# Optimization experiments

Hardware: AMD Instinct MI355X
Metric: run time of the kernel (lower is better)

Reference implementation:

```python
import jax, jax.numpy as jnp
import numpy as np
import math

B, S, D_MODEL, N_HEAD = 4, 2048, 1024, 16
D_K = D_MODEL // N_HEAD
ROPE_THETA = 10000.0


def _rope(x):
    # x: [B, H, S, Dk]; interleaved-pair rotary embedding.
    b, h, s, d = x.shape
    inv_freq = ROPE_THETA ** (-jnp.arange(0, d, 2, dtype=jnp.float32) / d)  # [d/2]
    ang = jnp.arange(s, dtype=jnp.float32)[:, None] * inv_freq[None, :]      # [S, d/2]
    cos, sin = jnp.cos(ang), jnp.sin(ang)
    x1, x2 = x[..., 0::2], x[..., 1::2]
    r1 = x1 * cos - x2 * sin
    r2 = x1 * sin + x2 * cos
    return jnp.stack([r1, r2], axis=-1).reshape(b, h, s, d)


def setup_inputs() -> dict:
    key = jax.random.key(0)
    ks = jax.random.split(key, 7)
    sc = 1.0 / math.sqrt(D_MODEL)
    return {
        "q": jax.random.normal(ks[0], (B, S, D_MODEL), jnp.float32),
        "k": jax.random.normal(ks[1], (B, S, D_MODEL), jnp.float32),
        "v": jax.random.normal(ks[2], (B, S, D_MODEL), jnp.float32),
        "Wq": jax.random.normal(ks[3], (D_MODEL, D_MODEL), jnp.float32) * sc,
        "Wk": jax.random.normal(ks[4], (D_MODEL, D_MODEL), jnp.float32) * sc,
        "Wv": jax.random.normal(ks[5], (D_MODEL, D_MODEL), jnp.float32) * sc,
        "Wo": jax.random.normal(ks[6], (D_MODEL, D_MODEL), jnp.float32) * sc,
    }


def _split(x):
    b, s, d = x.shape
    return x.reshape(b, s, N_HEAD, d // N_HEAD).transpose(0, 2, 1, 3)  # [B,H,S,Dk]


def reference(q, k, v, Wq, Wk, Wv, Wo):
    q = jnp.einsum("bsd,de->bse", q, Wq)
    k = jnp.einsum("bsd,de->bse", k, Wk)
    v = jnp.einsum("bsd,de->bse", v, Wv)
    qh, kh, vh = _split(q), _split(k), _split(v)
    qh, kh = _rope(qh), _rope(kh)
    scale = 1.0 / math.sqrt(D_K)
    score = jnp.einsum("bhqd,bhkd->bhqk", qh, kh) * scale  # [B,H,S,S]
    attn = jax.nn.softmax(score, axis=-1)
    out = jnp.einsum("bhqk,bhkd->bhqd", attn, vh)
    out = out.transpose(0, 2, 1, 3).reshape(q.shape[0], q.shape[1], D_MODEL)
    return jnp.einsum("bsd,de->bse", out, Wo)
```

## Files before the change

### kernel.cpp

```cpp
#include <hip/hip_runtime.h>
#include <stdint.h>

#define Bv 4
#define Sv 2048
#define Dv 1024
#define Hv 16
#define DKv 64
#define BSv (Bv * Sv)

typedef unsigned short u16;
typedef __attribute__((ext_vector_type(8))) short short8;
typedef __attribute__((ext_vector_type(8))) unsigned short u16x8;
typedef __attribute__((ext_vector_type(4))) unsigned short u16x4;
typedef __attribute__((ext_vector_type(4))) float f32x4;
typedef __attribute__((ext_vector_type(16))) float f32x16;

__device__ __forceinline__ u16 f2bf(float f) {
  union { float f; uint32_t u; } x; x.f = f;
  uint32_t r = x.u + 0x7FFFu + ((x.u >> 16) & 1u);
  return (u16)(r >> 16);
}

__device__ __forceinline__ uint32_t cvtpk(float lo, float hi) {
  uint32_t r;
  asm("v_cvt_pk_bf16_f32 %0, %1, %2" : "=v"(r) : "v"(lo), "v"(hi));
  return r;
}

__device__ __forceinline__ void gl_lds16(const void* g, void* l) {
  __builtin_amdgcn_global_load_lds(
      (__attribute__((address_space(1))) void*)g,
      (__attribute__((address_space(3))) void*)l, 16, 0, 0);
}

__device__ __forceinline__ f32x4 mfma16(short8 a, short8 b, f32x4 c) {
  return __builtin_amdgcn_mfma_f32_16x16x32_bf16(a, b, c, 0, 0, 0);
}
__device__ __forceinline__ f32x16 mfma32(short8 a, short8 b, f32x16 c) {
  return __builtin_amdgcn_mfma_f32_32x32x16_bf16(a, b, c, 0, 0, 0);
}

template <int N>
__device__ __forceinline__ void tsync() {
  asm volatile("s_waitcnt vmcnt(%0) lgkmcnt(0)" ::"n"(N) : "memory");
  __builtin_amdgcn_s_barrier();
  __builtin_amdgcn_sched_barrier(0);
}

__global__ __launch_bounds__(256) void conv_wt(
    const float* __restrict__ w0, const float* __restrict__ w1,
    const float* __restrict__ w2, const float* __restrict__ w3,
    u16* __restrict__ t0, u16* __restrict__ t1, u16* __restrict__ t2,
    u16* __restrict__ t3) {
  const float* W = (blockIdx.z == 0) ? w0 : (blockIdx.z == 1 ? w1 : (blockIdx.z == 2 ? w2 : w3));
  u16* T = (blockIdx.z == 0) ? t0 : (blockIdx.z == 1 ? t1 : (blockIdx.z == 2 ? t2 : t3));
  __shared__ u16 tile[64][72];
  int nb = blockIdx.x * 64, kb = blockIdx.y * 64;
  int t = threadIdx.x;
#pragma unroll
  for (int p = 0; p < 4; ++p) {
    int idx = p * 256 + t;
    int r = idx >> 4;
    int c4 = (idx & 15) * 4;
    float4 vv = *(const float4*)(W + (size_t)(kb + r) * Dv + nb + c4);
    tile[c4 + 0][r] = f2bf(vv.x);
    tile[c4 + 1][r] = f2bf(vv.y);
    tile[c4 + 2][r] = f2bf(vv.z);
    tile[c4 + 3][r] = f2bf(vv.w);
  }
  __syncthreads();
#pragma unroll
  for (int p = 0; p < 4; ++p) {
    int idx = p * 256 + t;
    int r = idx >> 4;
    int c4 = (idx & 15) * 4;
    u16x4 o = { tile[r][c4], tile[r][c4 + 1], tile[r][c4 + 2], tile[r][c4 + 3] };
    *(u16x4*)(T + (size_t)(nb + r) * Dv + kb + c4) = o;
  }
}

__global__ __launch_bounds__(256, 2) void gemm_qkv(
    const float* __restrict__ A0, const float* __restrict__ A1, const float* __restrict__ A2,
    const u16* __restrict__ B0, const u16* __restrict__ B1, const u16* __restrict__ B2,
    u16* __restrict__ O0, u16* __restrict__ O1, u16* __restrict__ O2) {
  __shared__ u16 As[2][128 * 64];
  __shared__ u16 Bs[2][128 * 64];
  int z = blockIdx.z;
  const float* A = (z == 0) ? A0 : (z == 1 ? A1 : A2);
  const u16* Bt  = (z == 0) ? B0 : (z == 1 ? B1 : B2);
  u16* Out       = (z == 0) ? O0 : (z == 1 ? O1 : O2);
  int mode = z;

  int tid = threadIdx.x;
  int lane = tid & 63, wid = tid >> 6;
  int quad = lane >> 4, cc = lane & 15;
  int wm = (wid >> 1) * 64, wn = (wid & 1) * 64;
  int m0 = blockIdx.x * 128, n0 = blockIdx.y * 128;

  f32x4 acc[4][4];
#pragma unroll
  for (int mi = 0; mi < 4; ++mi)
#pragma unroll
    for (int ni = 0; ni < 4; ++ni) {
      f32x4 zf = {0.f, 0.f, 0.f, 0.f};
      acc[mi][ni] = zf;
    }

  auto stageB = [&](int ki, int b) {
#pragma unroll
    for (int p = 0; p < 4; ++p) {
      int slot = p * 256 + tid;
      int row = slot >> 3, cl = slot & 7;
      int cg = cl ^ (row & 7);
      gl_lds16(Bt + (size_t)(n0 + row) * Dv + ki * 64 + cg * 8, &Bs[b][slot * 8]);
    }
  };

  float4 fa0[4][2], fa1[4][2];
  auto loadA = [&](int ki, float4 (&fs)[4][2]) {
#pragma unroll
    for (int p = 0; p < 4; ++p) {
      int slot = p * 256 + tid;
      int row = slot >> 3, cl = slot & 7;
      int cg = cl ^ (row & 7);
      const float* g = A + (size_t)(m0 + row) * Dv + ki * 64 + cg * 8;
      fs[p][0] = *(const float4*)g;
      fs[p][1] = *(const float4*)(g + 4);
    }
  };
  auto writeA = [&](int b, const float4 (&fs)[4][2]) {
#pragma unroll
    for (int p = 0; p < 4; ++p) {
      int slot = p * 256 + tid;
      union { uint32_t u[4]; u16x8 s; } o;
      o.u[0] = cvtpk(fs[p][0].x, fs[p][0].y);
      o.u[1] = cvtpk(fs[p][0].z, fs[p][0].w);
      o.u[2] = cvtpk(fs[p][1].x, fs[p][1].y);
      o.u[3] = cvtpk(fs[p][1].z, fs[p][1].w);
      *(u16x8*)&As[b][slot * 8] = o.s;
    }
  };
  auto computeTile = [&](int cur) {
#pragma unroll
    for (int kk = 0; kk < 2; ++kk) {
      short8 af[4], bfr[4];
#pragma unroll
      for (int mi = 0; mi < 4; ++mi) {
        int row = wm + mi * 16 + cc;
        int cg = kk * 4 + quad;
        af[mi] = *(const short8*)&As[cur][row * 64 + (cg ^ (row & 7)) * 8];
      }
#pragma unroll
      for (int ni = 0; ni < 4; ++ni) {
        int row = wn + ni * 16 + cc;
        int cg = kk * 4 + quad;
        bfr[ni] = *(const short8*)&Bs[cur][row * 64 + (cg ^ (row & 7)) * 8];
      }
#pragma unroll
      for (int mi = 0; mi < 4; ++mi)
#pragma unroll
        for (int ni = 0; ni < 4; ++ni)
          acc[mi][ni] = mfma16(af[mi], bfr[ni], acc[mi][ni]);
    }
  };

  loadA(0, fa0); writeA(0, fa0); stageB(0, 0);
  asm volatile("" ::: "memory");
  loadA(1, fa1);

  const int NT = Dv / 64;
#pragma unroll 1
  for (int tt = 0; tt < NT; tt += 2) {
    tsync<8>();
    if (tt + 1 < NT) stageB(tt + 1, 1);
    asm volatile("" ::: "memory");
    if (tt + 2 < NT) loadA(tt + 2, fa0);
    computeTile(0);
    if (tt + 1 < NT) writeA(1, fa1);
    if (tt + 2 < NT) tsync<8>(); else tsync<0>();
    if (tt + 2 < NT) stageB(tt + 2, 0);
    asm volatile("" ::: "memory");
    if (tt + 3 < NT) loadA(tt + 3, fa1);
    computeTile(1);
    if (tt + 2 < NT) writeA(0, fa0);
  }

  if (mode <= 1) {
    float postscale = (mode == 0) ? 0.18033688011112042f : 1.0f;
#pragma unroll
    for (int ni = 0; ni < 4; ++ni) {
      int n = n0 + wn + ni * 16 + cc;
      int h = n >> 6, d = n & 63;
      float inv = __expf(-(float)(d & 62) * (9.210340372f / 64.0f));
      float sign = (d & 1) ? 1.0f : -1.0f;
#pragma unroll
      for (int mi = 0; mi < 4; ++mi) {
        int mB = m0 + wm + mi * 16 + quad * 4;
#pragma unroll
        for (int r = 0; r < 4; ++r) {
          int m = mB + r;
          int b = m >> 11, s = m & (Sv - 1);
          float val = acc[mi][ni][r];
          float part = __shfl_xor(val, 1);
          float sn, cs;
          __sincosf((float)s * inv, &sn, &cs);
          float outv = (val * cs + sign * part * sn) * postscale;
          Out[((size_t)(b * Hv + h) * Sv + s) * DKv + d] = f2bf(outv);
        }
      }
    }
  } else {
#pragma unroll
    for (int ni = 0; ni < 4; ++ni) {
      int n = n0 + wn + ni * 16 + cc;
      int h = n >> 6, d = n & 63;
#pragma unroll
      for (int mi = 0; mi < 4; ++mi) {
        int mB = m0 + wm + mi * 16 + quad * 4;
        int b = mB >> 11, s = mB & (Sv - 1);
        u16x4 o4 = { f2bf(acc[mi][ni][0]), f2bf(acc[mi][ni][1]),
                     f2bf(acc[mi][ni][2]), f2bf(acc[mi][ni][3]) };
        *(u16x4*)&Out[((size_t)(b * Hv + h) * DKv + d) * Sv + s] = o4;
      }
    }
  }
}

__global__ __launch_bounds__(256) void gemm_out(
    const u16* __restrict__ A, const u16* __restrict__ Bt,
    float* __restrict__ O) {
  __shared__ u16 As[2][128 * 64];
  __shared__ u16 Bs[2][128 * 64];

  int tid = threadIdx.x;
  int lane = tid & 63, wid = tid >> 6;
  int quad = lane >> 4, cc = lane & 15;
  int wm = (wid >> 1) * 64, wn = (wid & 1) * 64;
  int m0 = blockIdx.x * 128, n0 = blockIdx.y * 128;

  f32x4 acc[4][4];
#pragma unroll
  for (int mi = 0; mi < 4; ++mi)
#pragma unroll
    for (int ni = 0; ni < 4; ++ni) {
      f32x4 zf = {0.f, 0.f, 0.f, 0.f};
      acc[mi][ni] = zf;
    }

#pragma unroll
  for (int p = 0; p < 4; ++p) {
    int slot = p * 256 + tid;
    int row = slot >> 3, cl = slot & 7;
    int cg = cl ^ (row & 7);
    gl_lds16(A + (size_t)(m0 + row) * Dv + cg * 8, &As[0][slot * 8]);
    gl_lds16(Bt + (size_t)(n0 + row) * Dv + cg * 8, &Bs[0][slot * 8]);
  }

  for (int ki = 0; ki < Dv / 64; ++ki) {
    int cur = ki & 1;
    __syncthreads();

    if (ki + 1 < Dv / 64) {
      int k1 = (ki + 1) * 64;
#pragma unroll
      for (int p = 0; p < 4; ++p) {
        int slot = p * 256 + tid;
        int row = slot >> 3, cl = slot & 7;
        int cg = cl ^ (row & 7);
        gl_lds16(A + (size_t)(m0 + row) * Dv + k1 + cg * 8, &As[1 - cur][slot * 8]);
        gl_lds16(Bt + (size_t)(n0 + row) * Dv + k1 + cg * 8, &Bs[1 - cur][slot * 8]);
      }
    }

#pragma unroll
    for (int kk = 0; kk < 2; ++kk) {
      short8 af[4], bfr[4];
#pragma unroll
      for (int mi = 0; mi < 4; ++mi) {
        int row = wm + mi * 16 + cc;
        int cg = kk * 4 + quad;
        af[mi] = *(const short8*)&As[cur][row * 64 + (cg ^ (row & 7)) * 8];
      }
#pragma unroll
      for (int ni = 0; ni < 4; ++ni) {
        int row = wn + ni * 16 + cc;
        int cg = kk * 4 + quad;
        bfr[ni] = *(const short8*)&Bs[cur][row * 64 + (cg ^ (row & 7)) * 8];
      }
#pragma unroll
      for (int mi = 0; mi < 4; ++mi)
#pragma unroll
        for (int ni = 0; ni < 4; ++ni)
          acc[mi][ni] = mfma16(af[mi], bfr[ni], acc[mi][ni]);
    }
  }

#pragma unroll
  for (int ni = 0; ni < 4; ++ni) {
    int n = n0 + wn + ni * 16 + cc;
#pragma unroll
    for (int mi = 0; mi < 4; ++mi) {
      int mB = m0 + wm + mi * 16 + quad * 4;
#pragma unroll
      for (int r = 0; r < 4; ++r)
        O[(size_t)(mB + r) * Dv + n] = acc[mi][ni][r];
    }
  }
}

__global__ __launch_bounds__(256, 2) void attn(
    const u16* __restrict__ Qp, const u16* __restrict__ Kp,
    const u16* __restrict__ Vt, u16* __restrict__ ctx) {
  __shared__ u16 Ks[2][64 * 64];
  __shared__ u16 Vs[2][64 * 64];
  int tid = threadIdx.x;
  int lane = tid & 63, wid = tid >> 6;
  int hi = lane >> 5, c32 = lane & 31;
  int sz = (c32 & 7) ^ ((c32 >> 3) & 3);
  int bh = blockIdx.y;
  int q0 = blockIdx.x * 256 + wid * 64;
  const u16* Qh = Qp + (size_t)bh * Sv * DKv;
  const u16* Kh = Kp + (size_t)bh * Sv * DKv;
  const u16* Vh = Vt + (size_t)bh * Sv * DKv;

  const short8 ones = { (short)0x3F80, (short)0x3F80, (short)0x3F80, (short)0x3F80,
                        (short)0x3F80, (short)0x3F80, (short)0x3F80, (short)0x3F80 };

  short8 qf[2][4];
#pragma unroll
  for (int qs = 0; qs < 2; ++qs)
#pragma unroll
    for (int dk = 0; dk < 4; ++dk)
      qf[qs][dk] = *(const short8*)&Qh[(size_t)(q0 + qs * 32 + c32) * DKv + dk * 16 + hi * 8];

  f32x16 o[2][2];
  f32x16 ol[2];
#pragma unroll
  for (int qs = 0; qs < 2; ++qs) {
#pragma unroll
    for (int dt = 0; dt < 2; ++dt)
#pragma unroll
      for (int r = 0; r < 16; ++r) o[qs][dt][r] = 0.f;
#pragma unroll
    for (int r = 0; r < 16; ++r) ol[qs][r] = 0.f;
  }

#pragma unroll
  for (int p = 0; p < 2; ++p) {
    int slot = p * 256 + tid;
    int row = slot >> 3, cl = slot & 7;
    int cg = cl ^ ((row & 7) ^ ((row >> 3) & 3));
    gl_lds16(Kh + (size_t)row * DKv + cg * 8, &Ks[0][slot * 8]);
    gl_lds16(Vh + (size_t)row * Sv + cg * 8, &Vs[0][slot * 8]);
  }

  for (int kt = 0; kt < Sv / 64; ++kt) {
    int cur = kt & 1;
    __syncthreads();

    if (kt + 1 < Sv / 64) {
      int s1 = (kt + 1) * 64;
#pragma unroll
      for (int p = 0; p < 2; ++p) {
        int slot = p * 256 + tid;
        int row = slot >> 3, cl = slot & 7;
        int cg = cl ^ ((row & 7) ^ ((row >> 3) & 3));
        gl_lds16(Kh + (size_t)(s1 + row) * DKv + cg * 8, &Ks[1 - cur][slot * 8]);
        gl_lds16(Vh + (size_t)row * Sv + s1 + cg * 8, &Vs[1 - cur][slot * 8]);
      }
    }

#pragma unroll
    for (int half = 0; half < 2; ++half) {
      short8 kf[4];
#pragma unroll
      for (int dk = 0; dk < 4; ++dk)
        kf[dk] = *(const short8*)&Ks[cur][(half * 32 + c32) * 64 + (((dk * 2 + hi) ^ sz)) * 8];

      f32x16 st[2];
#pragma unroll
      for (int qs = 0; qs < 2; ++qs) {
#pragma unroll
        for (int r = 0; r < 16; ++r) st[qs][r] = 0.f;
#pragma unroll
        for (int dk = 0; dk < 4; ++dk)
          st[qs] = mfma32(kf[dk], qf[qs][dk], st[qs]);
      }

#pragma unroll
      for (int pp = 0; pp < 2; ++pp) {
        int pk = half * 2 + pp;
        short8 vf[2];
#pragma unroll
        for (int dt = 0; dt < 2; ++dt)
          vf[dt] = *(const short8*)&Vs[cur][(dt * 32 + c32) * 64 + (((pk * 2 + hi) ^ sz)) * 8];
#pragma unroll
        for (int qs = 0; qs < 2; ++qs) {
          float e0 = __builtin_amdgcn_exp2f(st[qs][8 * pp + 0]);
          float e1 = __builtin_amdgcn_exp2f(st[qs][8 * pp + 1]);
          float e2 = __builtin_amdgcn_exp2f(st[qs][8 * pp + 2]);
          float e3 = __builtin_amdgcn_exp2f(st[qs][8 * pp + 3]);
          float e4 = __builtin_amdgcn_exp2f(st[qs][8 * pp + 4]);
          float e5 = __builtin_amdgcn_exp2f(st[qs][8 * pp + 5]);
          float e6 = __builtin_amdgcn_exp2f(st[qs][8 * pp + 6]);
          float e7 = __builtin_amdgcn_exp2f(st[qs][8 * pp + 7]);
          uint32_t plo0 = __builtin_amdgcn_perm(__float_as_uint(e1), __float_as_uint(e0), 0x07060302u);
          uint32_t plo1 = __builtin_amdgcn_perm(__float_as_uint(e3), __float_as_uint(e2), 0x07060302u);
          uint32_t phi0 = __builtin_amdgcn_perm(__float_as_uint(e5), __float_as_uint(e4), 0x07060302u);
          uint32_t phi1 = __builtin_amdgcn_perm(__float_as_uint(e7), __float_as_uint(e6), 0x07060302u);
          uint32_t s0 = hi ? plo0 : phi0;
          uint32_t s1 = hi ? plo1 : phi1;
          uint32_t r0 = (uint32_t)__shfl_xor((int)s0, 32);
          uint32_t r1 = (uint32_t)__shfl_xor((int)s1, 32);
          union { uint32_t u[4]; short8 s8; } pu;
          pu.u[0] = hi ? r0 : plo0;
          pu.u[1] = hi ? r1 : plo1;
          pu.u[2] = hi ? phi0 : r0;
          pu.u[3] = hi ? phi1 : r1;
          ol[qs] = mfma32(pu.s8, ones, ol[qs]);
          o[qs][0] = mfma32(pu.s8, vf[0], o[qs][0]);
          o[qs][1] = mfma32(pu.s8, vf[1], o[qs][1]);
        }
      }
    }
  }

  int b = bh >> 4, h = bh & 15;
#pragma unroll
  for (int qs = 0; qs < 2; ++qs)
#pragma unroll
    for (int r = 0; r < 16; ++r) {
      int q = q0 + qs * 32 + (r & 3) + 8 * (r >> 2) + 4 * hi;
      float linv = 1.0f / ol[qs][r];
#pragma unroll
      for (int dt = 0; dt < 2; ++dt) {
        int d = h * DKv + dt * 32 + c32;
        ctx[((size_t)b * Sv + q) * Dv + d] = f2bf(o[qs][dt][r] * linv);
      }
    }
}

extern "C" void kernel_launch(void* const* d_in, const int* in_sizes, int n_in,
                              void* d_out, int out_size, void* d_ws, size_t ws_size,
                              hipStream_t stream) {
  (void)in_sizes; (void)n_in; (void)out_size; (void)ws_size;
  const float* q  = (const float*)d_in[0];
  const float* k  = (const float*)d_in[1];
  const float* v  = (const float*)d_in[2];
  const float* Wq = (const float*)d_in[3];
  const float* Wk = (const float*)d_in[4];
  const float* Wv = (const float*)d_in[5];
  const float* Wo = (const float*)d_in[6];

  char* ws = (char*)d_ws;
  size_t off = 0;
  const size_t big = (size_t)BSv * Dv * sizeof(u16);
  const size_t wsz = (size_t)Dv * Dv * sizeof(u16);
  u16* Wqt = (u16*)(ws + off); off += wsz;
  u16* Wkt = (u16*)(ws + off); off += wsz;
  u16* Wvt = (u16*)(ws + off); off += wsz;
  u16* Wot = (u16*)(ws + off); off += wsz;
  u16* Qp  = (u16*)(ws + off); off += big;
  u16* Kp  = (u16*)(ws + off); off += big;
  u16* Vtr = (u16*)(ws + off); off += big;
  u16* ctx = (u16*)(ws + off); off += big;

  conv_wt<<<dim3(Dv / 64, Dv / 64, 4), 256, 0, stream>>>(Wq, Wk, Wv, Wo, Wqt, Wkt, Wvt, Wot);
  gemm_qkv<<<dim3(BSv / 128, Dv / 128, 3), 256, 0, stream>>>(
      q, k, v, Wqt, Wkt, Wvt, Qp, Kp, Vtr);
  attn<<<dim3(Sv / 256, Bv * Hv), 256, 0, stream>>>(Qp, Kp, Vtr, ctx);
  gemm_out<<<dim3(BSv / 128, Dv / 128), 256, 0, stream>>>(ctx, Wot, (float*)d_out);
}
```

Before: 325.5 us.

## Restructure QKV GEMM to 256x128 tiles with 8 waves and triple-buffered B

Measured after the change: 335.6 us. 1.03x slower.

```diff
diff --git a/kernel.cpp b/kernel.cpp
--- a/kernel.cpp
+++ b/kernel.cpp
@@ -40,6 +40,13 @@
   return __builtin_amdgcn_mfma_f32_32x32x16_bf16(a, b, c, 0, 0, 0);
 }
 
+__device__ __forceinline__ void fence() { asm volatile("" ::: "memory"); }
+
+__device__ __forceinline__ void bar() {
+  asm volatile("" ::: "memory");
+  __builtin_amdgcn_s_barrier();
+  asm volatile("" ::: "memory");
+}
 template <int N>
 __device__ __forceinline__ void tsync() {
   asm volatile("s_waitcnt vmcnt(%0) lgkmcnt(0)" ::"n"(N) : "memory");
@@ -79,12 +86,12 @@
   }
 }
 
-__global__ __launch_bounds__(256, 2) void gemm_qkv(
+__global__ __launch_bounds__(512, 1) void gemm_qkv(
     const float* __restrict__ A0, const float* __restrict__ A1, const float* __restrict__ A2,
     const u16* __restrict__ B0, const u16* __restrict__ B1, const u16* __restrict__ B2,
     u16* __restrict__ O0, u16* __restrict__ O1, u16* __restrict__ O2) {
-  __shared__ u16 As[2][128 * 64];
-  __shared__ u16 Bs[2][128 * 64];
+  __shared__ u16 As[2][256 * 64];
+  __shared__ u16 Bs[3][128 * 64];
   int z = blockIdx.z;
   const float* A = (z == 0) ? A0 : (z == 1 ? A1 : A2);
   const u16* Bt  = (z == 0) ? B0 : (z == 1 ? B1 : B2);
@@ -95,7 +102,9 @@
   int lane = tid & 63, wid = tid >> 6;
   int quad = lane >> 4, cc = lane & 15;
   int wm = (wid >> 1) * 64, wn = (wid & 1) * 64;
-  int m0 = blockIdx.x * 128, n0 = blockIdx.y * 128;
+  int bx = blockIdx.x;
+  int swz = (bx & 7) * 32 + (bx >> 3);
+  int m0 = (swz >> 3) * 256, n0 = (swz & 7) * 128;
 
   f32x4 acc[4][4];
 #pragma unroll
@@ -106,21 +115,19 @@
       acc[mi][ni] = zf;
     }
 
-  auto stageB = [&](int ki, int b) {
-#pragma unroll
-    for (int p = 0; p < 4; ++p) {
-      int slot = p * 256 + tid;
-      int row = slot >> 3, cl = slot & 7;
-      int cg = cl ^ (row & 7);
-      gl_lds16(Bt + (size_t)(n0 + row) * Dv + ki * 64 + cg * 8, &Bs[b][slot * 8]);
-    }
+  auto stageB1 = [&](int ki, int b, int p0) {
+    int slot = p0 * 512 + tid;
+    int row = slot >> 3, cl = slot & 7;
+    int cg = cl ^ (row & 7);
+    gl_lds16(Bt + (size_t)(n0 + row) * Dv + ki * 64 + cg * 8, &Bs[b][slot * 8]);
   };
 
   float4 fa0[4][2], fa1[4][2];
-  auto loadA = [&](int ki, float4 (&fs)[4][2]) {
-#pragma unroll
-    for (int p = 0; p < 4; ++p) {
-      int slot = p * 256 + tid;
+  auto loadA2 = [&](int ki, float4 (&fs)[4][2], int p0) {
+#pragma unroll
+    for (int pp = 0; pp < 2; ++pp) {
+      int p = p0 + pp;
+      int slot = p * 512 + tid;
       int row = slot >> 3, cl = slot & 7;
       int cg = cl ^ (row & 7);
       const float* g = A + (size_t)(m0 + row) * Dv + ki * 64 + cg * 8;
@@ -131,7 +138,7 @@
   auto writeA = [&](int b, const float4 (&fs)[4][2]) {
 #pragma unroll
     for (int p = 0; p < 4; ++p) {
-      int slot = p * 256 + tid;
+      int slot = p * 512 + tid;
       union { uint32_t u[4]; u16x8 s; } o;
       o.u[0] = cvtpk(fs[p][0].x, fs[p][0].y);
       o.u[1] = cvtpk(fs[p][0].z, fs[p][0].w);
@@ -140,49 +147,75 @@
       *(u16x8*)&As[b][slot * 8] = o.s;
     }
   };
-  auto computeTile = [&](int cur) {
-#pragma unroll
-    for (int kk = 0; kk < 2; ++kk) {
-      short8 af[4], bfr[4];
-#pragma unroll
-      for (int mi = 0; mi < 4; ++mi) {
-        int row = wm + mi * 16 + cc;
-        int cg = kk * 4 + quad;
-        af[mi] = *(const short8*)&As[cur][row * 64 + (cg ^ (row & 7)) * 8];
-      }
-#pragma unroll
-      for (int ni = 0; ni < 4; ++ni) {
-        int row = wn + ni * 16 + cc;
-        int cg = kk * 4 + quad;
-        bfr[ni] = *(const short8*)&Bs[cur][row * 64 + (cg ^ (row & 7)) * 8];
-      }
-#pragma unroll
-      for (int mi = 0; mi < 4; ++mi)
-#pragma unroll
-        for (int ni = 0; ni < 4; ++ni)
-          acc[mi][ni] = mfma16(af[mi], bfr[ni], acc[mi][ni]);
-    }
+
+  const int NT = Dv / 64;
+  int cur3 = 0, nxt3 = 2;
+
+  auto body = [&](int t, int curA, float4 (&fld)[4][2], const float4 (&fwr)[4][2]) {
+    const u16* Ac = &As[curA][0];
+    const u16* Bc = &Bs[cur3][0];
+    short8 af[4], bfr[4];
+#pragma unroll
+    for (int mi = 0; mi < 4; ++mi) {
+      int row = wm + mi * 16 + cc;
+      af[mi] = *(const short8*)&Ac[row * 64 + ((0 * 4 + quad) ^ (row & 7)) * 8];
+    }
+#pragma unroll
+    for (int ni = 0; ni < 4; ++ni) {
+      int row = wn + ni * 16 + cc;
+      bfr[ni] = *(const short8*)&Bc[row * 64 + ((0 * 4 + quad) ^ (row & 7)) * 8];
+    }
+    if (t + 2 < NT) { stageB1(t + 2, nxt3, 0); fence(); loadA2(t + 2, fld, 0); }
+    bar();
+    __builtin_amdgcn_s_setprio(1);
+#pragma unroll
+    for (int mi = 0; mi < 4; ++mi)
+#pragma unroll
+      for (int ni = 0; ni < 4; ++ni)
+        acc[mi][ni] = mfma16(af[mi], bfr[ni], acc[mi][ni]);
+    __builtin_amdgcn_s_setprio(0);
+    bar();
+#pragma unroll
+    for (int mi = 0; mi < 4; ++mi) {
+      int row = wm + mi * 16 + cc;
+      af[mi] = *(const short8*)&Ac[row * 64 + ((1 * 4 + quad) ^ (row & 7)) * 8];
+    }
+#pragma unroll
+    for (int ni = 0; ni < 4; ++ni) {
+      int row = wn + ni * 16 + cc;
+      bfr[ni] = *(const short8*)&Bc[row * 64 + ((1 * 4 + quad) ^ (row & 7)) * 8];
+    }
+    if (t + 2 < NT) { stageB1(t + 2, nxt3, 1); fence(); loadA2(t + 2, fld, 2); }
+    bar();
+    __builtin_amdgcn_s_setprio(1);
+#pragma unroll
+    for (int mi = 0; mi < 4; ++mi)
+#pragma unroll
+      for (int ni = 0; ni < 4; ++ni)
+        acc[mi][ni] = mfma16(af[mi], bfr[ni], acc[mi][ni]);
+    __builtin_amdgcn_s_setprio(0);
+    if (t + 1 < NT) writeA(1 - curA, fwr);
+    if (t < NT - 1) {
+      if (t + 2 < NT) tsync<10>(); else tsync<0>();
+    }
+    cur3 = (cur3 == 2) ? 0 : cur3 + 1;
+    nxt3 = (nxt3 == 2) ? 0 : nxt3 + 1;
   };
 
-  loadA(0, fa0); writeA(0, fa0); stageB(0, 0);
-  asm volatile("" ::: "memory");
-  loadA(1, fa1);
-
-  const int NT = Dv / 64;
+  loadA2(0, fa0, 0); loadA2(0, fa0, 2);
+  writeA(0, fa0);
+  fence();
+  stageB1(0, 0, 0); stageB1(0, 0, 1);
+  fence();
+  stageB1(1, 1, 0); stageB1(1, 1, 1);
+  fence();
+  loadA2(1, fa1, 0); loadA2(1, fa1, 2);
+  tsync<10>();
+
 #pragma unroll 1
   for (int tt = 0; tt < NT; tt += 2) {
-    tsync<8>();
-    if (tt + 1 < NT) stageB(tt + 1, 1);
-    asm volatile("" ::: "memory");
-    if (tt + 2 < NT) loadA(tt + 2, fa0);
-    computeTile(0);
-    if (tt + 1 < NT) writeA(1, fa1);
-    if (tt + 2 < NT) tsync<8>(); else tsync<0>();
-    if (tt + 2 < NT) stageB(tt + 2, 0);
-    asm volatile("" ::: "memory");
-    if (tt + 3 < NT) loadA(tt + 3, fa1);
-    computeTile(1);
-    if (tt + 2 < NT) writeA(0, fa0);
+    body(tt, 0, fa0, fa1);
+    body(tt + 1, 1, fa1, fa0);
   }
 
   if (mode <= 1) {
@@ -466,7 +499,7 @@
   u16* ctx = (u16*)(ws + off); off += big;
 
   conv_wt<<<dim3(Dv / 64, Dv / 64, 4), 256, 0, stream>>>(Wq, Wk, Wv, Wo, Wqt, Wkt, Wvt, Wot);
-  gemm_qkv<<<dim3(BSv / 128, Dv / 128, 3), 256, 0, stream>>>(
+  gemm_qkv<<<dim3(256, 1, 3), 512, 0, stream>>>(
       q, k, v, Wqt, Wkt, Wvt, Qp, Kp, Vtr);
   attn<<<dim3(Sv / 256, Bv * Hv), 256, 0, stream>>>(Qp, Kp, Vtr, ctx);
   gemm_out<<<dim3(BSv / 128, Dv / 128), 256, 0, stream>>>(ctx, Wot, (float*)d_out);
```
